# Kernel tuning notes

Hardware: AMD Instinct MI355X
Metric: run time of the kernel (lower is better)

The kernel has to match this reference:

```python
import jax, jax.numpy as jnp
import numpy as np

MAX_LEN = 4096
HEAD_DIM = 128
NUM_HEAD = 32
NUM_KV_GROUPS = 8
NUM_HEAD_KV = NUM_HEAD // NUM_KV_GROUPS
BASE = 10000.0


def _rope_tables(seq_len):
    pos = jnp.arange(seq_len, dtype=jnp.float32)
    freq = BASE ** (-(jnp.arange(0, HEAD_DIM, 2, dtype=jnp.float32) / HEAD_DIM))
    ang = pos[:, None] * freq[None, :]  # [n, d/2]
    return jnp.cos(ang), jnp.sin(ang)


def _apply_rope(x, cos, sin):
    # x: [..., n, d]; interleaved even/odd rotation as in the torch RoPe
    even = x[..., ::2]
    odd = x[..., 1::2]
    even_r = even * cos - odd * sin
    odd_r = odd * cos + even * sin
    return jnp.stack([even_r, odd_r], axis=-1).reshape(x.shape)


def setup_inputs() -> dict:
    key = jax.random.key(0)
    ks = jax.random.split(key, 9)
    B, N, D = 4, 1024, NUM_HEAD * HEAD_DIM
    KV = NUM_HEAD_KV * HEAD_DIM
    s = 0.02
    return {
        "x": jax.random.normal(ks[0], (B, N, D), jnp.float32),
        "Wq": jax.random.normal(ks[1], (D, D), jnp.float32) * s,
        "bq": jax.random.normal(ks[2], (D,), jnp.float32) * s,
        "Wk": jax.random.normal(ks[3], (D, KV), jnp.float32) * s,
        "bk": jax.random.normal(ks[4], (KV,), jnp.float32) * s,
        "Wv": jax.random.normal(ks[5], (D, KV), jnp.float32) * s,
        "bv": jax.random.normal(ks[6], (KV,), jnp.float32) * s,
        "Wo": jax.random.normal(ks[7], (D, D), jnp.float32) * s,
        "bo": jax.random.normal(ks[8], (D,), jnp.float32) * s,
    }


def reference(x, Wq, bq, Wk, bk, Wv, bv, Wo, bo):
    B, N, _ = x.shape
    g, h, d = NUM_KV_GROUPS, NUM_HEAD_KV, HEAD_DIM
    scale = d ** (-0.5)

    q = x @ Wq + bq                      # [B, N, g*h*d]
    k = x @ Wk + bk                      # [B, N, h*d]
    v = x @ Wv + bv

    # b n (g h d) -> b g h n d (group-major, matching einops pattern)
    q = q.reshape(B, N, g, h, d).transpose(0, 2, 3, 1, 4)
    k = k.reshape(B, N, h, d).transpose(0, 2, 1, 3)   # b h n d
    v = v.reshape(B, N, h, d).transpose(0, 2, 1, 3)

    cos, sin = _rope_tables(N)
    q = _apply_rope(q, cos, sin)
    k = _apply_rope(k, cos, sin)

    attn = jnp.einsum('bghid,bhjd->bghij', q * scale, k)
    causal = jnp.tril(jnp.ones((N, N), dtype=bool))
    attn = jnp.where(causal, attn, -jnp.inf)
    attn = jax.nn.softmax(attn, axis=-1)

    out = jnp.einsum('bghij,bhjd->bghid', attn, v)
    out = out.transpose(0, 3, 1, 2, 4).reshape(B, N, g * h * d)  # b g h n d -> b n (g h d)
    return out @ Wo + bo
```

## Files before the change

### kernel.cpp

```cpp
#include <hip/hip_runtime.h>
#include <cstdint>
#include <cstddef>

typedef unsigned short u16;
typedef unsigned int u32;

typedef __bf16 bf16x8 __attribute__((ext_vector_type(8)));
typedef float f32x4 __attribute__((ext_vector_type(4)));
typedef u16 u16x8 __attribute__((ext_vector_type(8)));

__device__ __forceinline__ u16 f2bf(float f) {
  union { float f; u32 u; } v; v.f = f;
  u32 r = v.u + 0x7fffu + ((v.u >> 16) & 1u);
  return (u16)(r >> 16);
}
__device__ __forceinline__ float bf2f(u16 h) {
  union { u32 u; float f; } v; v.u = ((u32)h) << 16;
  return v.f;
}

__device__ __forceinline__ void gld16(const u16* g, u16* l) {
  __builtin_amdgcn_global_load_lds((const __attribute__((address_space(1))) u32*)g,
                                   (__attribute__((address_space(3))) u32*)l,
                                   16, 0, 0);
}

template<bool OUT_F32>
__global__ __launch_bounds__(256)
void gemm_bt(const u16* __restrict__ A, const u16* __restrict__ Bt,
             const float* __restrict__ bias, void* __restrict__ C,
             int M, int N, int K) {
  __shared__ __attribute__((aligned(16))) u16 As[2][128*32];
  __shared__ __attribute__((aligned(16))) u16 Bs[2][128*32];
  const int tid  = threadIdx.x;
  const int lane = tid & 63;
  const int wave = tid >> 6;
  const int wm = wave >> 1, wn = wave & 1;
  const int bn = blockIdx.x * 128;
  const int bm = blockIdx.y * 128;
  const int kq = lane >> 4, ml = lane & 15;

  const u16* agp[2]; const u16* bgp[2]; int ldst[2];
#pragma unroll
  for (int j = 0; j < 2; ++j) {
    int s = wave*128 + j*64 + lane;
    int r = s >> 2;
    int c = (s & 3) ^ ((r >> 1) & 3);
    agp[j] = A  + (size_t)(bm + r)*K + c*8;
    bgp[j] = Bt + (size_t)(bn + r)*K + c*8;
    ldst[j] = (wave*128 + j*64)*8;
  }

  auto stage = [&](int p, int k0) {
#pragma unroll
    for (int j = 0; j < 2; ++j) {
      gld16(agp[j] + k0, &As[p][0] + ldst[j]);
      gld16(bgp[j] + k0, &Bs[p][0] + ldst[j]);
    }
  };

  f32x4 acc[4][4] = {};

  auto compute = [&](int p) {
    bf16x8 af[4], bfr[4];
#pragma unroll
    for (int t = 0; t < 4; ++t) {
      int ra = wm*64 + t*16 + ml;
      af[t]  = *(const bf16x8*)(&As[p][0] + (size_t)(ra*4 + (kq ^ ((ra >> 1) & 3)))*8);
      int rb = wn*64 + t*16 + ml;
      bfr[t] = *(const bf16x8*)(&Bs[p][0] + (size_t)(rb*4 + (kq ^ ((rb >> 1) & 3)))*8);
    }
#pragma unroll
    for (int i = 0; i < 4; ++i)
#pragma unroll
      for (int j = 0; j < 4; ++j)
        acc[i][j] = __builtin_amdgcn_mfma_f32_16x16x32_bf16(af[i], bfr[j], acc[i][j], 0, 0, 0);
  };

  stage(0, 0);
  for (int k0 = 0; k0 < K; k0 += 64) {
    __syncthreads();
    if (k0 + 32 < K) stage(1, k0 + 32);
    compute(0);
    __syncthreads();
    if (k0 + 64 < K) stage(0, k0 + 64);
    compute(1);
  }

#pragma unroll
  for (int i = 0; i < 4; ++i) {
    int rg0 = bm + wm*64 + i*16 + kq*4;
#pragma unroll
    for (int j = 0; j < 4; ++j) {
      int cg = bn + wn*64 + j*16 + ml;
      float bv = bias[cg];
#pragma unroll
      for (int r = 0; r < 4; ++r) {
        float v = acc[i][j][r] + bv;
        if (OUT_F32) ((float*)C)[(size_t)(rg0 + r)*N + cg] = v;
        else         ((u16*)C)[(size_t)(rg0 + r)*N + cg]   = f2bf(v);
      }
    }
  }
}

__global__ __launch_bounds__(256)
void attn(const u16* __restrict__ Q, const u16* __restrict__ K,
          const u16* __restrict__ V, u16* __restrict__ ctx) {
  __shared__ __attribute__((aligned(16))) u16 Qs[64*128];
  __shared__ __attribute__((aligned(16))) u16 Ks[64*128];
  __shared__ __attribute__((aligned(16))) u16 Vs[128*64];
  __shared__ __attribute__((aligned(16))) u16 Ps[4][16*72];
  const int qt  = (int)gridDim.x - 1 - (int)blockIdx.x;
  const int bh  = blockIdx.y;
  const int b   = bh >> 5;
  const int kvh = bh & 3;
  const int tid = threadIdx.x;
  const int lane = tid & 63;
  const int wave = tid >> 6;
  const int kq = lane >> 4, ml = lane & 15;

  const u16* Qg = Q + ((size_t)bh*1024 + qt*64)*128;
  const u16* Kg = K + ((size_t)(b*4 + kvh))*1024*128;
  const u16* Vg = V + ((size_t)(b*4 + kvh))*128*1024;

#pragma unroll
  for (int j = 0; j < 4; ++j) {
    int s = wave*256 + j*64 + lane;
    int r = s >> 4, c = (s & 15) ^ (r & 7);
    gld16(Qg + (size_t)r*128 + c*8, Qs + (size_t)(wave*256 + j*64)*8);
  }

  f32x4 o[8] = {};
  float m_i[4] = {-1e30f, -1e30f, -1e30f, -1e30f};
  float l_i[4] = {0.f, 0.f, 0.f, 0.f};

  for (int kt = 0; kt <= qt; ++kt) {
    __syncthreads();
#pragma unroll
    for (int j = 0; j < 4; ++j) {
      int s = wave*256 + j*64 + lane;
      int r = s >> 4, c = (s & 15) ^ (r & 7);
      gld16(Kg + ((size_t)(kt*64 + r))*128 + c*8, Ks + (size_t)(wave*256 + j*64)*8);
    }
#pragma unroll
    for (int j = 0; j < 4; ++j) {
      int s = wave*256 + j*64 + lane;
      int d = s >> 3, c = (s & 7) ^ (d & 7);
      gld16(Vg + (size_t)d*1024 + kt*64 + c*8, Vs + (size_t)(wave*256 + j*64)*8);
    }
    __syncthreads();

    f32x4 sf[4] = {};
#pragma unroll
    for (int ks = 0; ks < 4; ++ks) {
      int rq = wave*16 + ml;
      int cq = ks*4 + kq;
      bf16x8 aq = *(const bf16x8*)(Qs + (size_t)(rq*16 + (cq ^ (rq & 7)))*8);
#pragma unroll
      for (int nt = 0; nt < 4; ++nt) {
        int rk = nt*16 + ml;
        bf16x8 bk = *(const bf16x8*)(Ks + (size_t)(rk*16 + (cq ^ (rk & 7)))*8);
        sf[nt] = __builtin_amdgcn_mfma_f32_16x16x32_bf16(aq, bk, sf[nt], 0, 0, 0);
      }
    }

    const int i0 = qt*64 + wave*16 + kq*4;
    if (kt == qt) {
#pragma unroll
      for (int nt = 0; nt < 4; ++nt) {
        int jg = kt*64 + nt*16 + ml;
#pragma unroll
        for (int r = 0; r < 4; ++r)
          if (jg > i0 + r) sf[nt][r] = -1e30f;
      }
    }
    float rmax[4] = {-1e30f, -1e30f, -1e30f, -1e30f};
#pragma unroll
    for (int nt = 0; nt < 4; ++nt)
#pragma unroll
      for (int r = 0; r < 4; ++r)
        rmax[r] = fmaxf(rmax[r], sf[nt][r]);
#pragma unroll
    for (int r = 0; r < 4; ++r) {
      float v = rmax[r];
      v = fmaxf(v, __shfl_xor(v, 1));
      v = fmaxf(v, __shfl_xor(v, 2));
      v = fmaxf(v, __shfl_xor(v, 4));
      v = fmaxf(v, __shfl_xor(v, 8));
      float mo = m_i[r];
      float mn = fmaxf(mo, v);
      m_i[r] = mn;
      rmax[r] = exp2f(mo - mn);
    }
    float rsum[4] = {0.f, 0.f, 0.f, 0.f};
#pragma unroll
    for (int nt = 0; nt < 4; ++nt)
#pragma unroll
      for (int r = 0; r < 4; ++r) {
        float p = exp2f(sf[nt][r] - m_i[r]);
        rsum[r] += p;
        Ps[wave][(kq*4 + r)*72 + nt*16 + ml] = f2bf(p);
      }
#pragma unroll
    for (int r = 0; r < 4; ++r) {
      float v = rsum[r];
      v += __shfl_xor(v, 1);
      v += __shfl_xor(v, 2);
      v += __shfl_xor(v, 4);
      v += __shfl_xor(v, 8);
      l_i[r] = l_i[r]*rmax[r] + v;
    }
#pragma unroll
    for (int dt = 0; dt < 8; ++dt)
#pragma unroll
      for (int r = 0; r < 4; ++r)
        o[dt][r] *= rmax[r];
    __syncthreads();

#pragma unroll
    for (int ks = 0; ks < 2; ++ks) {
      bf16x8 ap = *(const bf16x8*)(&Ps[wave][ml*72 + ks*32 + kq*8]);
#pragma unroll
      for (int dt = 0; dt < 8; ++dt) {
        int dv = dt*16 + ml;
        int cv = ks*4 + kq;
        bf16x8 bv = *(const bf16x8*)(Vs + (size_t)(dv*8 + (cv ^ (dv & 7)))*8);
        o[dt] = __builtin_amdgcn_mfma_f32_16x16x32_bf16(ap, bv, o[dt], 0, 0, 0);
      }
    }
  }

  const int head = bh & 31;
  float inv[4];
#pragma unroll
  for (int r = 0; r < 4; ++r) inv[r] = 1.f / l_i[r];
  size_t row0 = (size_t)b*1024 + qt*64 + wave*16 + kq*4;
#pragma unroll
  for (int dt = 0; dt < 8; ++dt) {
    int cg = head*128 + dt*16 + ml;
#pragma unroll
    for (int r = 0; r < 4; ++r)
      ctx[(row0 + r)*4096 + cg] = f2bf(o[dt][r]*inv[r]);
  }
}

__global__ void castx(const float* __restrict__ x, u16* __restrict__ xb) {
  size_t i = ((size_t)blockIdx.x*256 + threadIdx.x)*4;
  float4 v = *(const float4*)(x + i);
  ushort4 o; o.x = f2bf(v.x); o.y = f2bf(v.y); o.z = f2bf(v.z); o.w = f2bf(v.w);
  *(ushort4*)(xb + i) = o;
}

__global__ void wtrans(const float* __restrict__ W, u16* __restrict__ Wt, int K, int N) {
  __shared__ u16 t[64*71 + 8];
  const int n0 = blockIdx.x*64, k0 = blockIdx.y*64;
  const int tid = threadIdx.x;
  const int kr = tid >> 4, nc = (tid & 15)*4;
#pragma unroll
  for (int i = 0; i < 4; ++i) {
    float4 v = *(const float4*)(W + (size_t)(k0 + kr + i*16)*N + n0 + nc);
    u16* d = &t[(kr + i*16)*71 + nc];
    d[0] = f2bf(v.x); d[1] = f2bf(v.y); d[2] = f2bf(v.z); d[3] = f2bf(v.w);
  }
  __syncthreads();
  const int n = tid >> 2, k16 = (tid & 3)*16;
  u16x8 lo, hi;
#pragma unroll
  for (int j = 0; j < 8; ++j) lo[j] = t[(k16 + j)*71 + n];
#pragma unroll
  for (int j = 0; j < 8; ++j) hi[j] = t[(k16 + 8 + j)*71 + n];
  u16* dst = Wt + (size_t)(n0 + n)*K + k0 + k16;
  *(u16x8*)(dst)     = lo;
  *(u16x8*)(dst + 8) = hi;
}

__global__ void packbias(const float* __restrict__ bq, const float* __restrict__ bk,
                         const float* __restrict__ bv, float* __restrict__ out) {
  int i = blockIdx.x*256 + threadIdx.x;
  float v;
  if (i < 4096)      v = bq[i];
  else if (i < 4608) v = bk[i - 4096];
  else               v = bv[i - 4608];
  out[i] = v;
}

__global__ void rope_q(const u16* __restrict__ qkv, u16* __restrict__ qr) {
  int idx = blockIdx.x*256 + threadIdx.x;
  int dp = idx & 63;
  int head = (idx >> 6) & 31;
  int n = (idx >> 11) & 1023;
  int b = idx >> 21;
  const u16* src = qkv + ((size_t)(b*1024 + n))*5120 + head*128 + dp*2;
  float e = bf2f(src[0]), od = bf2f(src[1]);
  float freq = exp2f((float)dp * -0.2076205059f);
  float ang = (float)n * freq;
  float c = cosf(ang), s = sinf(ang);
  const float QS = 0.12751747f;
  u16* dst = qr + (((size_t)(b*32 + head))*1024 + n)*128 + dp*2;
  dst[0] = f2bf((e*c - od*s)*QS);
  dst[1] = f2bf((od*c + e*s)*QS);
}

__global__ void rope_k(const u16* __restrict__ qkv, u16* __restrict__ kr) {
  int idx = blockIdx.x*256 + threadIdx.x;
  int dp = idx & 63;
  int kvh = (idx >> 6) & 3;
  int n = (idx >> 8) & 1023;
  int b = idx >> 18;
  const u16* src = qkv + ((size_t)(b*1024 + n))*5120 + 4096 + kvh*128 + dp*2;
  float e = bf2f(src[0]), od = bf2f(src[1]);
  float freq = exp2f((float)dp * -0.2076205059f);
  float ang = (float)n * freq;
  float c = cosf(ang), s = sinf(ang);
  u16* dst = kr + (((size_t)(b*4 + kvh))*1024 + n)*128 + dp*2;
  dst[0] = f2bf(e*c - od*s);
  dst[1] = f2bf(od*c + e*s);
}

__global__ void vtrans(const u16* __restrict__ qkv, u16* __restrict__ vt) {
  __shared__ u16 t[32][40];
  const int nt = blockIdx.x, dt = blockIdx.y, bk = blockIdx.z;
  const int b = bk >> 2, kvh = bk & 3;
  const int tid = threadIdx.x;
  const int r = tid >> 3, c4 = (tid & 7)*4;
  const u16* src = qkv + ((size_t)(b*1024 + nt*32 + r))*5120 + 4608 + kvh*128 + dt*32 + c4;
#pragma unroll
  for (int i = 0; i < 4; ++i) t[r][c4 + i] = src[i];
  __syncthreads();
  u16* dst = vt + ((size_t)((b*4 + kvh)*128 + dt*32 + r))*1024 + nt*32 + c4;
#pragma unroll
  for (int i = 0; i < 4; ++i) dst[i] = t[c4 + i][r];
}

extern "C" void kernel_launch(void* const* d_in, const int* in_sizes, int n_in,
                              void* d_out, int out_size, void* d_ws, size_t ws_size,
                              hipStream_t stream) {
  const float* x  = (const float*)d_in[0];
  const float* Wq = (const float*)d_in[1];
  const float* bq = (const float*)d_in[2];
  const float* Wk = (const float*)d_in[3];
  const float* bk = (const float*)d_in[4];
  const float* Wv = (const float*)d_in[5];
  const float* bv = (const float*)d_in[6];
  const float* Wo = (const float*)d_in[7];
  const float* bo = (const float*)d_in[8];
  float* out = (float*)d_out;

  char* ws = (char*)d_ws;
  u16*   xb   = (u16*)(ws + 0);
  u16*   wqkv = (u16*)(ws + 33554432);
  u16*   wo_t = (u16*)(ws + 75497472);
  float* bqkv = (float*)(ws + 109051904);
  u16*   qkvl = (u16*)(ws + 109072384);
  u16*   qr   = (u16*)(ws + 33554432);
  u16*   kr   = (u16*)(ws + 67108864);
  u16*   vt   = (u16*)(ws + 71303168);
  u16*   ctx  = (u16*)(ws + 0);

  castx<<<16384, 256, 0, stream>>>(x, xb);
  wtrans<<<dim3(64,64), 256, 0, stream>>>(Wq, wqkv, 4096, 4096);
  wtrans<<<dim3(8,64),  256, 0, stream>>>(Wk, wqkv + (size_t)4096*4096, 4096, 512);
  wtrans<<<dim3(8,64),  256, 0, stream>>>(Wv, wqkv + (size_t)4608*4096, 4096, 512);
  wtrans<<<dim3(64,64), 256, 0, stream>>>(Wo, wo_t, 4096, 4096);
  packbias<<<20, 256, 0, stream>>>(bq, bk, bv, bqkv);

  gemm_bt<false><<<dim3(40,32), 256, 0, stream>>>(xb, wqkv, bqkv, qkvl, 4096, 5120, 4096);

  rope_q<<<32768, 256, 0, stream>>>(qkvl, qr);
  rope_k<<<4096,  256, 0, stream>>>(qkvl, kr);
  vtrans<<<dim3(32,4,16), 256, 0, stream>>>(qkvl, vt);

  attn<<<dim3(16,128), 256, 0, stream>>>(qr, kr, vt, ctx);

  gemm_bt<true><<<dim3(32,32), 256, 0, stream>>>(ctx, wo_t, bo, out, 4096, 4096, 4096);
}
```

Before: 838.8 us.

## Replace LDS-direct loads with register-staged prefetch in GEMM and attention

The GEMM and attention kernels stop using global_load_lds. They now prefetch the next K/V or A/B tiles into registers while the current tile computes, then store them to swizzled LDS, and the __syncthreads calls become raw s_barrier / s_waitcnt sequences. Attention keeps Q fragments in registers instead of LDS, and the RoPE kernels use the fast __sincosf. This aims to overlap global latency with MFMA work, but it raises register pressure. The fast sincos also loses accuracy for large angles (n up to 1023).

```diff
diff --git a/kernel.cpp b/kernel.cpp
--- a/kernel.cpp
+++ b/kernel.cpp
@@ -19,10 +19,11 @@
   return v.f;
 }
 
-__device__ __forceinline__ void gld16(const u16* g, u16* l) {
-  __builtin_amdgcn_global_load_lds((const __attribute__((address_space(1))) u32*)g,
-                                   (__attribute__((address_space(3))) u32*)l,
-                                   16, 0, 0);
+__device__ __forceinline__ void bar_lgkm() {
+  asm volatile("s_waitcnt lgkmcnt(0)\n\ts_barrier" ::: "memory");
+}
+__device__ __forceinline__ void bar_only() {
+  asm volatile("s_barrier" ::: "memory");
 }
 
 template<bool OUT_F32>
@@ -40,24 +41,20 @@
   const int bm = blockIdx.y * 128;
   const int kq = lane >> 4, ml = lane & 15;
 
-  const u16* agp[2]; const u16* bgp[2]; int ldst[2];
-#pragma unroll
-  for (int j = 0; j < 2; ++j) {
-    int s = wave*128 + j*64 + lane;
-    int r = s >> 2;
-    int c = (s & 3) ^ ((r >> 1) & 3);
-    agp[j] = A  + (size_t)(bm + r)*K + c*8;
-    bgp[j] = Bt + (size_t)(bn + r)*K + c*8;
-    ldst[j] = (wave*128 + j*64)*8;
-  }
-
-  auto stage = [&](int p, int k0) {
-#pragma unroll
-    for (int j = 0; j < 2; ++j) {
-      gld16(agp[j] + k0, &As[p][0] + ldst[j]);
-      gld16(bgp[j] + k0, &Bs[p][0] + ldst[j]);
-    }
-  };
+  const int ci0 = tid * 2;
+  const int r0  = ci0 >> 2, c0 = ci0 & 3;
+  const u16* agA = A  + (size_t)(bm + r0)*K + c0*8;
+  const u16* agB = Bt + (size_t)(bn + r0)*K + c0*8;
+  const int sw  = (r0 >> 1) & 3;
+  const int s0  = (r0*4 + (c0 ^ sw))*8;
+  const int s1  = (r0*4 + ((c0+1) ^ sw))*8;
+
+  uint4 a00, a01, b00, b01;
+  uint4 a10, a11, b10, b11;
+  a00 = *(const uint4*)(agA + 0);  a01 = *(const uint4*)(agA + 8);
+  b00 = *(const uint4*)(agB + 0);  b01 = *(const uint4*)(agB + 8);
+  a10 = *(const uint4*)(agA + 32); a11 = *(const uint4*)(agA + 40);
+  b10 = *(const uint4*)(agB + 32); b11 = *(const uint4*)(agB + 40);
 
   f32x4 acc[4][4] = {};
 
@@ -77,13 +74,22 @@
         acc[i][j] = __builtin_amdgcn_mfma_f32_16x16x32_bf16(af[i], bfr[j], acc[i][j], 0, 0, 0);
   };
 
-  stage(0, 0);
   for (int k0 = 0; k0 < K; k0 += 64) {
-    __syncthreads();
-    if (k0 + 32 < K) stage(1, k0 + 32);
+    *(uint4*)(&As[0][s0]) = a00;  *(uint4*)(&As[0][s1]) = a01;
+    *(uint4*)(&Bs[0][s0]) = b00;  *(uint4*)(&Bs[0][s1]) = b01;
+    if (k0 + 64 < K) {
+      a00 = *(const uint4*)(agA + k0 + 64); a01 = *(const uint4*)(agA + k0 + 72);
+      b00 = *(const uint4*)(agB + k0 + 64); b01 = *(const uint4*)(agB + k0 + 72);
+    }
+    bar_lgkm();
     compute(0);
-    __syncthreads();
-    if (k0 + 64 < K) stage(0, k0 + 64);
+    *(uint4*)(&As[1][s0]) = a10;  *(uint4*)(&As[1][s1]) = a11;
+    *(uint4*)(&Bs[1][s0]) = b10;  *(uint4*)(&Bs[1][s1]) = b11;
+    if (k0 + 96 < K) {
+      a10 = *(const uint4*)(agA + k0 + 96);  a11 = *(const uint4*)(agA + k0 + 104);
+      b10 = *(const uint4*)(agB + k0 + 96);  b11 = *(const uint4*)(agB + k0 + 104);
+    }
+    bar_lgkm();
     compute(1);
   }
 
@@ -107,7 +113,6 @@
 __global__ __launch_bounds__(256)
 void attn(const u16* __restrict__ Q, const u16* __restrict__ K,
           const u16* __restrict__ V, u16* __restrict__ ctx) {
-  __shared__ __attribute__((aligned(16))) u16 Qs[64*128];
   __shared__ __attribute__((aligned(16))) u16 Ks[64*128];
   __shared__ __attribute__((aligned(16))) u16 Vs[128*64];
   __shared__ __attribute__((aligned(16))) u16 Ps[4][16*72];
@@ -120,15 +125,24 @@
   const int wave = tid >> 6;
   const int kq = lane >> 4, ml = lane & 15;
 
-  const u16* Qg = Q + ((size_t)bh*1024 + qt*64)*128;
   const u16* Kg = K + ((size_t)(b*4 + kvh))*1024*128;
   const u16* Vg = V + ((size_t)(b*4 + kvh))*128*1024;
 
-#pragma unroll
-  for (int j = 0; j < 4; ++j) {
-    int s = wave*256 + j*64 + lane;
-    int r = s >> 4, c = (s & 15) ^ (r & 7);
-    gld16(Qg + (size_t)r*128 + c*8, Qs + (size_t)(wave*256 + j*64)*8);
+  const u16* Qrow = Q + ((size_t)bh*1024 + qt*64 + wave*16 + ml)*128;
+  bf16x8 aq[4];
+#pragma unroll
+  for (int ks = 0; ks < 4; ++ks)
+    aq[ks] = *(const bf16x8*)(Qrow + ks*32 + kq*8);
+
+  const int kr0 = tid >> 2, kc0 = (tid & 3)*4;
+  const int vd0 = tid >> 1, vc0 = (tid & 1)*4;
+  const u16* kgp = Kg + (size_t)kr0*128 + kc0*8;
+  const u16* vgp = Vg + (size_t)vd0*1024 + vc0*8;
+  uint4 krg[4], vrg[4];
+#pragma unroll
+  for (int i = 0; i < 4; ++i) {
+    krg[i] = *(const uint4*)(kgp + i*8);
+    vrg[i] = *(const uint4*)(vgp + i*8);
   }
 
   f32x4 o[8] = {};
@@ -136,32 +150,30 @@
   float l_i[4] = {0.f, 0.f, 0.f, 0.f};
 
   for (int kt = 0; kt <= qt; ++kt) {
-    __syncthreads();
-#pragma unroll
-    for (int j = 0; j < 4; ++j) {
-      int s = wave*256 + j*64 + lane;
-      int r = s >> 4, c = (s & 15) ^ (r & 7);
-      gld16(Kg + ((size_t)(kt*64 + r))*128 + c*8, Ks + (size_t)(wave*256 + j*64)*8);
-    }
-#pragma unroll
-    for (int j = 0; j < 4; ++j) {
-      int s = wave*256 + j*64 + lane;
-      int d = s >> 3, c = (s & 7) ^ (d & 7);
-      gld16(Vg + (size_t)d*1024 + kt*64 + c*8, Vs + (size_t)(wave*256 + j*64)*8);
-    }
-    __syncthreads();
+    bar_only();
+#pragma unroll
+    for (int i = 0; i < 4; ++i) {
+      *(uint4*)(&Ks[(size_t)(kr0*16 + ((kc0+i) ^ (kr0 & 7)))*8]) = krg[i];
+      *(uint4*)(&Vs[(size_t)(vd0*8  + ((vc0+i) ^ (vd0 & 7)))*8]) = vrg[i];
+    }
+    if (kt < qt) {
+#pragma unroll
+      for (int i = 0; i < 4; ++i) {
+        krg[i] = *(const uint4*)(kgp + (size_t)(kt+1)*64*128 + i*8);
+        vrg[i] = *(const uint4*)(vgp + (size_t)(kt+1)*64 + i*8);
+      }
+    }
+    bar_lgkm();
 
     f32x4 sf[4] = {};
 #pragma unroll
     for (int ks = 0; ks < 4; ++ks) {
-      int rq = wave*16 + ml;
       int cq = ks*4 + kq;
-      bf16x8 aq = *(const bf16x8*)(Qs + (size_t)(rq*16 + (cq ^ (rq & 7)))*8);
 #pragma unroll
       for (int nt = 0; nt < 4; ++nt) {
         int rk = nt*16 + ml;
         bf16x8 bk = *(const bf16x8*)(Ks + (size_t)(rk*16 + (cq ^ (rk & 7)))*8);
-        sf[nt] = __builtin_amdgcn_mfma_f32_16x16x32_bf16(aq, bk, sf[nt], 0, 0, 0);
+        sf[nt] = __builtin_amdgcn_mfma_f32_16x16x32_bf16(aq[ks], bk, sf[nt], 0, 0, 0);
       }
     }
 
@@ -216,7 +228,6 @@
 #pragma unroll
       for (int r = 0; r < 4; ++r)
         o[dt][r] *= rmax[r];
-    __syncthreads();
 
 #pragma unroll
     for (int ks = 0; ks < 2; ++ks) {
@@ -295,7 +306,8 @@
   float e = bf2f(src[0]), od = bf2f(src[1]);
   float freq = exp2f((float)dp * -0.2076205059f);
   float ang = (float)n * freq;
-  float c = cosf(ang), s = sinf(ang);
+  float s, c;
+  __sincosf(ang, &s, &c);
   const float QS = 0.12751747f;
   u16* dst = qr + (((size_t)(b*32 + head))*1024 + n)*128 + dp*2;
   dst[0] = f2bf((e*c - od*s)*QS);
@@ -312,7 +324,8 @@
   float e = bf2f(src[0]), od = bf2f(src[1]);
   float freq = exp2f((float)dp * -0.2076205059f);
   float ang = (float)n * freq;
-  float c = cosf(ang), s = sinf(ang);
+  float s, c;
+  __sincosf(ang, &s, &c);
   u16* dst = kr + (((size_t)(b*4 + kvh))*1024 + n)*128 + dp*2;
   dst[0] = f2bf(e*c - od*s);
   dst[1] = f2bf(od*c + e*s);
```

New measurement: 922.1 us. 9.9% more time.
